# Kernel tuning notes

Measured on AMD Instinct MI355X. Metric: run time of the kernel, lower is better.

## Reference

```python
import math
import jax, jax.numpy as jnp
import numpy as np

C, B, T, D = 8, 4, 8192, 64
MAX_LEN = 8192
_DELTA = math.log2(MAX_LEN) / max(C - 1, 1)
# lam_c = 1 - 2^{-(c*delta)}; lam_0 == 0 (memoryless channel)
LAMBDAS = jnp.array([1.0 - 2.0 ** (-(c * _DELTA)) for c in range(C)], dtype=jnp.float32)


def setup_inputs() -> dict:
    key = jax.random.key(0)
    k0, k1, k2 = jax.random.split(key, 3)
    return {
        "channels": jax.random.normal(k0, (C, B, T, D), dtype=jnp.float32),
        "gw_fwd": jax.random.normal(k1, (C, D, D), dtype=jnp.float32) * 0.02,
        "gb_fwd": jnp.ones((C, D), dtype=jnp.float32),
        "gw_bwd": jax.random.normal(k2, (C, D, D), dtype=jnp.float32) * 0.02,
        "gb_bwd": jnp.ones((C, D), dtype=jnp.float32),
    }


def _fixed_decay_scan(lam, v):
    """h_t = lam * h_{t-1} + v_t over axis=1 (time); v: [B,T,D], lam scalar.
    For lam==0 this reduces to identity, matching the torch fast path."""
    a = jnp.full_like(v, lam)

    def combine(x, y):
        a1, b1 = x
        a2, b2 = y
        return (a1 * a2, a2 * b1 + b2)

    return jax.lax.associative_scan(combine, (a, v), axis=1)[1]


def _run_direction(channels, W, b):
    # torch Linear: y = x @ W.T + b, W is (out,in) -> einsum 'cbtd,ced->cbte'
    g = jax.nn.sigmoid(jnp.einsum('cbtd,ced->cbte', channels, W) + b[:, None, None, :])
    gated = g * channels
    return jax.vmap(_fixed_decay_scan)(LAMBDAS, gated)  # [C,B,T,D]


def reference(channels, gw_fwd, gb_fwd, gw_bwd, gb_bwd):
    fwd = _run_direction(channels, gw_fwd, gb_fwd)
    rev = channels[:, :, ::-1, :]
    bwd = _run_direction(rev, gw_bwd, gb_bwd)[:, :, ::-1, :]
    return fwd, bwd
```

## Files before the change

### kernel.cpp

```cpp
#include <hip/hip_runtime.h>
#include <cmath>
#include <cstdint>

typedef __attribute__((ext_vector_type(8))) short short8;
typedef __attribute__((ext_vector_type(4))) float f32x4;
typedef __attribute__((ext_vector_type(2))) unsigned int u32x2;

struct Lams { float v[8]; };

#define NC 8
#define NB 4
#define NT 8192
#define ND 64
#define CL 256
#define NP 2
#define NCHUNK 32
#define NKK 16
#define NBLK (2 * NC * NB * NKK)
#define NSLOT (2 * NC * NB * NCHUNK)
#define NWAVE 8
#define LDH 68

__device__ __forceinline__ uint32_t pk2(float lo, float hi) {
    uint32_t r;
    asm("v_cvt_pk_bf16_f32 %0, %1, %2" : "=v"(r) : "v"(lo), "v"(hi));
    return r;
}

__device__ __forceinline__ float bf2f(unsigned short s) {
    return __builtin_bit_cast(float, (uint32_t)s << 16);
}
__device__ __forceinline__ float bflo(uint32_t u) { return bf2f((unsigned short)(u & 0xFFFFu)); }
__device__ __forceinline__ float bfhi(uint32_t u) { return bf2f((unsigned short)(u >> 16)); }

__global__ __launch_bounds__(512, 4) void k1_fused(
    const float* __restrict__ x, const float* __restrict__ Wf,
    const float* __restrict__ bf, const float* __restrict__ Wb,
    const float* __restrict__ bb, float* __restrict__ out,
    int* __restrict__ flags, float* __restrict__ evals, Lams lams)
{
    __shared__ unsigned short xbuf[CL * LDH];
    __shared__ float ends_lds[2][NWAVE][ND];
    __shared__ float hprev_lds[2][ND];

    const int tid  = threadIdx.x;
    const int lane = tid & 63;
    const int w    = tid >> 6;

    int idx = blockIdx.x;
    const int kk  = idx & (NKK - 1); idx >>= 4;
    const int b   = idx & (NB - 1);  idx >>= 2;
    const int c   = idx & (NC - 1);  idx >>= 3;
    const int dir = idx;

    const float lam = lams.v[c];
    const float* W    = (dir ? Wb : Wf) + c * ND * ND;
    const float* bias = (dir ? bb : bf) + c * ND;
    const float* xb   = x + (size_t)(c * NB + b) * NT * ND;
    float* ob = out + (size_t)dir * (size_t)(NC*NB*NT*ND)
                    + (size_t)(c * NB + b) * NT * ND;
    const int seqbase = (int)(blockIdx.x >> 4) * NCHUNK;

    const int er = lane & 15;
    const int ks = lane >> 4;
    const int r0 = w * 32;

    auto STAGE = [&](int gc) {
        const int sr = lane >> 4;
        const int sc = (lane & 15) * 4;
        const int tr = gc * CL + r0 + sr;
        if (dir == 0) {
            const float* p = xb + (size_t)tr * ND + sc;
            #pragma unroll
            for (int q = 0; q < 8; ++q) {
                f32x4 v = *reinterpret_cast<const f32x4*>(p + (size_t)q * 4 * ND);
                u32x2 u = { pk2(v[0], v[1]), pk2(v[2], v[3]) };
                *reinterpret_cast<u32x2*>(&xbuf[(r0 + q*4 + sr) * LDH + sc]) = u;
            }
        } else {
            const float* p = xb + (size_t)(NT-1 - tr) * ND + sc;
            #pragma unroll
            for (int q = 0; q < 8; ++q) {
                f32x4 v = *reinterpret_cast<const f32x4*>(p - (size_t)q * 4 * ND);
                u32x2 u = { pk2(v[0], v[1]), pk2(v[2], v[3]) };
                *reinterpret_cast<u32x2*>(&xbuf[(r0 + q*4 + sr) * LDH + sc]) = u;
            }
        }
    };

    short8 bfrag[4][2];
    #pragma unroll
    for (int et = 0; et < 4; ++et) {
        const float* wr = W + (et*16 + er) * ND + ks * 8;
        #pragma unroll
        for (int kq = 0; kq < 2; ++kq) {
            f32x4 lo = *reinterpret_cast<const f32x4*>(wr + kq*32);
            f32x4 hi = *reinterpret_cast<const f32x4*>(wr + kq*32 + 4);
            union { short8 s8; uint32_t u[4]; } t;
            t.u[0] = pk2(lo[0], lo[1]); t.u[1] = pk2(lo[2], lo[3]);
            t.u[2] = pk2(hi[0], hi[1]); t.u[3] = pk2(hi[2], hi[3]);
            bfrag[et][kq] = t.s8;
        }
    }
    float bias_r[4];
    #pragma unroll
    for (int et = 0; et < 4; ++et) bias_r[et] = bias[et*16 + er];

    float lam32 = lam*lam; lam32*=lam32; lam32*=lam32; lam32*=lam32; lam32*=lam32;

    STAGE(kk);

    #pragma unroll 1
    for (int p = 0; p < NP; ++p) {
        const int P   = p & 1;
        const int g   = kk + NKK * p;
        const int tr0 = g * CL;

        #pragma unroll
        for (int u = 0; u < 2; ++u) {
            const int rl0 = r0 + u*16;
            short8 afrag[2];
            afrag[0] = *reinterpret_cast<const short8*>(&xbuf[(rl0 + er) * LDH + ks * 8]);
            afrag[1] = *reinterpret_cast<const short8*>(&xbuf[(rl0 + er) * LDH + 32 + ks * 8]);
            #pragma unroll
            for (int et = 0; et < 4; ++et) {
                f32x4 acc = {0.f, 0.f, 0.f, 0.f};
                acc = __builtin_amdgcn_mfma_f32_16x16x32_bf16(afrag[0], bfrag[et][0], acc, 0,0,0);
                acc = __builtin_amdgcn_mfma_f32_16x16x32_bf16(afrag[1], bfrag[et][1], acc, 0,0,0);
                const int col = et*16 + er;
                float gated[4];
                #pragma unroll
                for (int r = 0; r < 4; ++r) {
                    const int rl = rl0 + ks*4 + r;
                    float z  = acc[r] + bias_r[et];
                    float gg = __builtin_amdgcn_rcpf(1.0f + __expf(-z));
                    float xv = bf2f(xbuf[rl * LDH + col]);
                    gated[r] = gg * xv;
                }
                uint32_t p01 = pk2(gated[0], gated[1]);
                uint32_t p23 = pk2(gated[2], gated[3]);
                xbuf[(rl0 + ks*4 + 0) * LDH + col] = (unsigned short)(p01 & 0xFFFF);
                xbuf[(rl0 + ks*4 + 1) * LDH + col] = (unsigned short)(p01 >> 16);
                xbuf[(rl0 + ks*4 + 2) * LDH + col] = (unsigned short)(p23 & 0xFFFF);
                xbuf[(rl0 + ks*4 + 3) * LDH + col] = (unsigned short)(p23 >> 16);
            }
        }

        {
            float h = 0.f;
            #pragma unroll
            for (int i = 0; i < 32; ++i) {
                const int a = (r0 + i) * LDH + lane;
                float v = bf2f(xbuf[a]);
                h = fmaf(h, lam, v);
                xbuf[a] = (unsigned short)(pk2(h, h) & 0xFFFF);
            }
            ends_lds[P][w][lane] = h;
        }
        __syncthreads();

        if (w == NWAVE - 1) {
            float carryW = 0.f;
            #pragma unroll
            for (int j = 0; j < NWAVE - 1; ++j)
                carryW = fmaf(carryW, lam32, ends_lds[P][j][lane]);
            float E = fmaf(carryW, lam32, ends_lds[P][NWAVE-1][lane]);

            float Hprev = 0.f;
            if (c != 0) {
                const int slot = seqbase + g;
                __hip_atomic_store(&evals[(size_t)slot * ND + lane], E,
                                   __ATOMIC_RELAXED, __HIP_MEMORY_SCOPE_AGENT);
                asm volatile("s_waitcnt vmcnt(0)" ::: "memory");
                if (lane == 0)
                    __hip_atomic_store(&flags[slot], 1, __ATOMIC_RELAXED,
                                       __HIP_MEMORY_SCOPE_AGENT);
                if (g != 0) {
                    if (lane < g) {
                        while (__hip_atomic_load(&flags[seqbase + lane], __ATOMIC_RELAXED,
                                                 __HIP_MEMORY_SCOPE_AGENT) == 0)
                            __builtin_amdgcn_s_sleep(2);
                    }
                    asm volatile("" ::: "memory");
                    const float* eb = evals + (size_t)seqbase * ND;
                    float l1 = lam32*lam32; l1 *= l1; l1 *= l1;
                    float l4 = l1 * l1; l4 *= l4;
                    float Ph = 0.f;
                    int j = 0;
                    const int rem = g & 3;
                    for (; j < rem; ++j)
                        Ph = fmaf(Ph, l1, eb[(size_t)j * ND + lane]);
                    for (; j < g; j += 4) {
                        float e0 = eb[(size_t)(j+0) * ND + lane];
                        float e1 = eb[(size_t)(j+1) * ND + lane];
                        float e2 = eb[(size_t)(j+2) * ND + lane];
                        float e3 = eb[(size_t)(j+3) * ND + lane];
                        float t = fmaf(fmaf(fmaf(e0, l1, e1), l1, e2), l1, e3);
                        Ph = fmaf(Ph, l4, t);
                    }
                    Hprev = Ph;
                }
            }
            hprev_lds[P][lane] = Hprev;
        }
        __syncthreads();

        {
            const int sr = lane >> 4;
            const int dg = lane & 15;
            float carry4[4];
            #pragma unroll
            for (int j2 = 0; j2 < 4; ++j2) {
                const int d = dg*4 + j2;
                float cy = 0.f, pw = 1.f;
                for (int j = 0; j < w; ++j) {
                    cy = fmaf(cy, lam32, ends_lds[P][j][d]);
                    pw *= lam32;
                }
                carry4[j2] = fmaf(pw, hprev_lds[P][d], cy);
            }
            const float lam2 = lam * lam, lam4 = lam2 * lam2;
            float f = lam;
            for (int j = 0; j < sr; ++j) f *= lam;
            if (dir == 0) {
                float* pp = ob + (size_t)(tr0 + r0 + sr) * ND + dg*4;
                #pragma unroll
                for (int q = 0; q < 8; ++q) {
                    u32x2 hv = *reinterpret_cast<const u32x2*>(
                        &xbuf[(r0 + q*4 + sr) * LDH + dg*4]);
                    f32x4 o;
                    o[0] = fmaf(f, carry4[0], bflo(hv[0]));
                    o[1] = fmaf(f, carry4[1], bfhi(hv[0]));
                    o[2] = fmaf(f, carry4[2], bflo(hv[1]));
                    o[3] = fmaf(f, carry4[3], bfhi(hv[1]));
                    *reinterpret_cast<f32x4*>(pp + (size_t)q * 4 * ND) = o;
                    f *= lam4;
                }
            } else {
                float* pp = ob + (size_t)(NT-1 - (tr0 + r0 + sr)) * ND + dg*4;
                #pragma unroll
                for (int q = 0; q < 8; ++q) {
                    u32x2 hv = *reinterpret_cast<const u32x2*>(
                        &xbuf[(r0 + q*4 + sr) * LDH + dg*4]);
                    f32x4 o;
                    o[0] = fmaf(f, carry4[0], bflo(hv[0]));
                    o[1] = fmaf(f, carry4[1], bfhi(hv[0]));
                    o[2] = fmaf(f, carry4[2], bflo(hv[1]));
                    o[3] = fmaf(f, carry4[3], bfhi(hv[1]));
                    *reinterpret_cast<f32x4*>(pp - (size_t)q * 4 * ND) = o;
                    f *= lam4;
                }
            }
        }

        if (p + 1 < NP) {
            asm volatile("" ::: "memory");
            STAGE(kk + NKK * (p + 1));
        }
    }
}

extern "C" void kernel_launch(void* const* d_in, const int* in_sizes, int n_in,
                              void* d_out, int out_size, void* d_ws, size_t ws_size,
                              hipStream_t stream)
{
    const float* x  = (const float*)d_in[0];
    const float* Wf = (const float*)d_in[1];
    const float* bf = (const float*)d_in[2];
    const float* Wb = (const float*)d_in[3];
    const float* bb = (const float*)d_in[4];
    float* out = (float*)d_out;

    int*   flags = (int*)d_ws;
    float* evals = (float*)((char*)d_ws + 16384);

    Lams lams;
    const double delta = 13.0 / 7.0;
    for (int c = 0; c < 8; ++c)
        lams.v[c] = (float)(1.0 - pow(2.0, -(double)c * delta));

    hipMemsetAsync(flags, 0, NSLOT * 4, stream);

    dim3 grid(NBLK);
    k1_fused<<<grid, 512, 0, stream>>>(x, Wf, bf, Wb, bb, out, flags, evals, lams);
}
```

Baseline: 72.99 us.

## Double-buffer LDS staging and prefetch next chunk during cross-block carry wait

Doubles the LDS staging buffer and moves the load of the next chunk into the window where wave 7 waits on the cross-block carry chain. Waves 0-6 stage their own rows and wave 0 also stages wave 7's rows. Each block now handles four chunks instead of two, halving the grid. The aim is to hide global-load latency behind the serial carry wait, at the cost of doubled LDS per block (occupancy bound lowered to 2 blocks per CU) and fewer blocks in flight.

```diff
diff --git a/kernel.cpp b/kernel.cpp
--- a/kernel.cpp
+++ b/kernel.cpp
@@ -13,9 +13,9 @@
 #define NT 8192
 #define ND 64
 #define CL 256
-#define NP 2
+#define NP 4
 #define NCHUNK 32
-#define NKK 16
+#define NKK 8
 #define NBLK (2 * NC * NB * NKK)
 #define NSLOT (2 * NC * NB * NCHUNK)
 #define NWAVE 8
@@ -33,13 +33,13 @@
 __device__ __forceinline__ float bflo(uint32_t u) { return bf2f((unsigned short)(u & 0xFFFFu)); }
 __device__ __forceinline__ float bfhi(uint32_t u) { return bf2f((unsigned short)(u >> 16)); }
 
-__global__ __launch_bounds__(512, 4) void k1_fused(
+__global__ __launch_bounds__(512, 2) void k1_fused(
     const float* __restrict__ x, const float* __restrict__ Wf,
     const float* __restrict__ bf, const float* __restrict__ Wb,
     const float* __restrict__ bb, float* __restrict__ out,
     int* __restrict__ flags, float* __restrict__ evals, Lams lams)
 {
-    __shared__ unsigned short xbuf[CL * LDH];
+    __shared__ unsigned short xbuf[2][CL * LDH];
     __shared__ float ends_lds[2][NWAVE][ND];
     __shared__ float hprev_lds[2][ND];
 
@@ -48,7 +48,7 @@
     const int w    = tid >> 6;
 
     int idx = blockIdx.x;
-    const int kk  = idx & (NKK - 1); idx >>= 4;
+    const int kk  = idx & (NKK - 1); idx >>= 3;
     const int b   = idx & (NB - 1);  idx >>= 2;
     const int c   = idx & (NC - 1);  idx >>= 3;
     const int dir = idx;
@@ -59,23 +59,23 @@
     const float* xb   = x + (size_t)(c * NB + b) * NT * ND;
     float* ob = out + (size_t)dir * (size_t)(NC*NB*NT*ND)
                     + (size_t)(c * NB + b) * NT * ND;
-    const int seqbase = (int)(blockIdx.x >> 4) * NCHUNK;
+    const int seqbase = (int)(blockIdx.x >> 3) * NCHUNK;
 
     const int er = lane & 15;
     const int ks = lane >> 4;
     const int r0 = w * 32;
 
-    auto STAGE = [&](int gc) {
+    auto STAGE = [&](int B, int gc, int rb) {
         const int sr = lane >> 4;
         const int sc = (lane & 15) * 4;
-        const int tr = gc * CL + r0 + sr;
+        const int tr = gc * CL + rb + sr;
         if (dir == 0) {
             const float* p = xb + (size_t)tr * ND + sc;
             #pragma unroll
             for (int q = 0; q < 8; ++q) {
                 f32x4 v = *reinterpret_cast<const f32x4*>(p + (size_t)q * 4 * ND);
                 u32x2 u = { pk2(v[0], v[1]), pk2(v[2], v[3]) };
-                *reinterpret_cast<u32x2*>(&xbuf[(r0 + q*4 + sr) * LDH + sc]) = u;
+                *reinterpret_cast<u32x2*>(&xbuf[B][(rb + q*4 + sr) * LDH + sc]) = u;
             }
         } else {
             const float* p = xb + (size_t)(NT-1 - tr) * ND + sc;
@@ -83,7 +83,7 @@
             for (int q = 0; q < 8; ++q) {
                 f32x4 v = *reinterpret_cast<const f32x4*>(p - (size_t)q * 4 * ND);
                 u32x2 u = { pk2(v[0], v[1]), pk2(v[2], v[3]) };
-                *reinterpret_cast<u32x2*>(&xbuf[(r0 + q*4 + sr) * LDH + sc]) = u;
+                *reinterpret_cast<u32x2*>(&xbuf[B][(rb + q*4 + sr) * LDH + sc]) = u;
             }
         }
     };
@@ -108,7 +108,7 @@
 
     float lam32 = lam*lam; lam32*=lam32; lam32*=lam32; lam32*=lam32; lam32*=lam32;
 
-    STAGE(kk);
+    STAGE(0, kk, r0);
 
     #pragma unroll 1
     for (int p = 0; p < NP; ++p) {
@@ -120,8 +120,8 @@
         for (int u = 0; u < 2; ++u) {
             const int rl0 = r0 + u*16;
             short8 afrag[2];
-            afrag[0] = *reinterpret_cast<const short8*>(&xbuf[(rl0 + er) * LDH + ks * 8]);
-            afrag[1] = *reinterpret_cast<const short8*>(&xbuf[(rl0 + er) * LDH + 32 + ks * 8]);
+            afrag[0] = *reinterpret_cast<const short8*>(&xbuf[P][(rl0 + er) * LDH + ks * 8]);
+            afrag[1] = *reinterpret_cast<const short8*>(&xbuf[P][(rl0 + er) * LDH + 32 + ks * 8]);
             #pragma unroll
             for (int et = 0; et < 4; ++et) {
                 f32x4 acc = {0.f, 0.f, 0.f, 0.f};
@@ -134,15 +134,15 @@
                     const int rl = rl0 + ks*4 + r;
                     float z  = acc[r] + bias_r[et];
                     float gg = __builtin_amdgcn_rcpf(1.0f + __expf(-z));
-                    float xv = bf2f(xbuf[rl * LDH + col]);
+                    float xv = bf2f(xbuf[P][rl * LDH + col]);
                     gated[r] = gg * xv;
                 }
                 uint32_t p01 = pk2(gated[0], gated[1]);
                 uint32_t p23 = pk2(gated[2], gated[3]);
-                xbuf[(rl0 + ks*4 + 0) * LDH + col] = (unsigned short)(p01 & 0xFFFF);
-                xbuf[(rl0 + ks*4 + 1) * LDH + col] = (unsigned short)(p01 >> 16);
-                xbuf[(rl0 + ks*4 + 2) * LDH + col] = (unsigned short)(p23 & 0xFFFF);
-                xbuf[(rl0 + ks*4 + 3) * LDH + col] = (unsigned short)(p23 >> 16);
+                xbuf[P][(rl0 + ks*4 + 0) * LDH + col] = (unsigned short)(p01 & 0xFFFF);
+                xbuf[P][(rl0 + ks*4 + 1) * LDH + col] = (unsigned short)(p01 >> 16);
+                xbuf[P][(rl0 + ks*4 + 2) * LDH + col] = (unsigned short)(p23 & 0xFFFF);
+                xbuf[P][(rl0 + ks*4 + 3) * LDH + col] = (unsigned short)(p23 >> 16);
             }
         }
 
@@ -151,9 +151,9 @@
             #pragma unroll
             for (int i = 0; i < 32; ++i) {
                 const int a = (r0 + i) * LDH + lane;
-                float v = bf2f(xbuf[a]);
+                float v = bf2f(xbuf[P][a]);
                 h = fmaf(h, lam, v);
-                xbuf[a] = (unsigned short)(pk2(h, h) & 0xFFFF);
+                xbuf[P][a] = (unsigned short)(pk2(h, h) & 0xFFFF);
             }
             ends_lds[P][w][lane] = h;
         }
@@ -202,6 +202,10 @@
                 }
             }
             hprev_lds[P][lane] = Hprev;
+        } else if (p + 1 < NP) {
+            STAGE(P ^ 1, kk + NKK * (p + 1), r0);
+            if (w == 0)
+                STAGE(P ^ 1, kk + NKK * (p + 1), 7 * 32);
         }
         __syncthreads();
 
@@ -227,7 +231,7 @@
                 #pragma unroll
                 for (int q = 0; q < 8; ++q) {
                     u32x2 hv = *reinterpret_cast<const u32x2*>(
-                        &xbuf[(r0 + q*4 + sr) * LDH + dg*4]);
+                        &xbuf[P][(r0 + q*4 + sr) * LDH + dg*4]);
                     f32x4 o;
                     o[0] = fmaf(f, carry4[0], bflo(hv[0]));
                     o[1] = fmaf(f, carry4[1], bfhi(hv[0]));
@@ -241,7 +245,7 @@
                 #pragma unroll
                 for (int q = 0; q < 8; ++q) {
                     u32x2 hv = *reinterpret_cast<const u32x2*>(
-                        &xbuf[(r0 + q*4 + sr) * LDH + dg*4]);
+                        &xbuf[P][(r0 + q*4 + sr) * LDH + dg*4]);
                     f32x4 o;
                     o[0] = fmaf(f, carry4[0], bflo(hv[0]));
                     o[1] = fmaf(f, carry4[1], bfhi(hv[0]));
@@ -251,11 +255,6 @@
                     f *= lam4;
                 }
             }
-        }
-
-        if (p + 1 < NP) {
-            asm volatile("" ::: "memory");
-            STAGE(kk + NKK * (p + 1));
         }
     }
 }
```

Measured after the change: 73.40 us. About the same (+0.6%).
